# Optimization experiments

Measured on AMD Instinct MI355X. Metric: run time of the kernel, lower is better.

Reference implementation:

```python
import jax, jax.numpy as jnp
import numpy as np

B, N, DEG = 64, 512, 16        # graphs, nodes per graph, avg degree
C, HID = 10, 128               # input feat dim (== num_classes quirk), hidden
E = B * N * DEG                # total edges (fixed; pooling masks edges)


def _gcn(x, W, b, src, dst, emask, n):
    # PyG GCNConv: add self-loops, symmetric norm D^-1/2 (A+I) D^-1/2 (XW) + b
    h = x @ W
    deg = jax.ops.segment_sum(emask, dst, num_segments=n) + 1.0  # +1 self-loop
    dinv = jax.lax.rsqrt(deg)
    norm = dinv[src] * dinv[dst] * emask
    agg = jax.ops.segment_sum(h[src] * norm[:, None], dst, num_segments=n)
    return agg + h * (dinv * dinv)[:, None] + b  # self-loop term + bias


def _sag_pool(x, src, dst, emask, Wp, bp, n_per):
    # SAGPooling: score = tanh(GCN(x)); per-graph top-k (ratio=0.5); x' = x[perm]*score
    n = x.shape[0]
    score = jnp.tanh(_gcn(x, Wp, bp, src, dst, emask, n)[:, 0])
    k = n_per // 2
    vals, idx = jax.lax.top_k(score.reshape(B, n_per), k)  # [B,k]
    perm = (idx + (jnp.arange(B) * n_per)[:, None]).reshape(-1)
    xk = x[perm] * vals.reshape(-1)[:, None]
    # relabel edges; drop edges touching removed nodes via mask (fixed E)
    mapping = jnp.full((n,), -1, jnp.int32).at[perm].set(
        jnp.arange(B * k, dtype=jnp.int32))
    ns, nd = mapping[src], mapping[dst]
    nmask = emask * ((ns >= 0) & (nd >= 0)).astype(emask.dtype)
    return xk, jnp.maximum(ns, 0), jnp.maximum(nd, 0), nmask, k


def _readout(x, k):
    # global max pool || global mean pool (all kept nodes are real, no padding)
    xg = x.reshape(B, k, -1)
    return jnp.concatenate([xg.max(axis=1), xg.mean(axis=1)], axis=1)


def setup_inputs() -> dict:
    key = jax.random.key(0)
    ks = jax.random.split(key, 16)
    x = jax.random.normal(ks[0], (B * N, C), jnp.float32)
    off = jnp.repeat(jnp.arange(B, dtype=jnp.int32) * N, N * DEG)
    src = jax.random.randint(ks[1], (E,), 0, N, jnp.int32) + off
    dst = jax.random.randint(ks[2], (E,), 0, N, jnp.int32) + off
    p = lambda k, s: jax.random.normal(k, s, jnp.float32) * 0.05
    return {
        "x": x, "src": src, "dst": dst,
        "W1": p(ks[3], (C, HID)), "b1": jnp.zeros((HID,), jnp.float32),
        "W2": p(ks[4], (HID, HID)), "b2": jnp.zeros((HID,), jnp.float32),
        "W3": p(ks[5], (HID, HID)), "b3": jnp.zeros((HID,), jnp.float32),
        "Wp": p(ks[6], (HID, 1)), "bp": jnp.zeros((1,), jnp.float32),
        "L1W": p(ks[7], (2 * HID, HID)), "L1b": jnp.zeros((HID,), jnp.float32),
        "L2W": p(ks[8], (HID, HID // 2)), "L2b": jnp.zeros((HID // 2,), jnp.float32),
    }


def reference(x, src, dst, W1, b1, W2, b2, W3, b3, Wp, bp, L1W, L1b, L2W, L2b):
    emask = jnp.ones((E,), jnp.float32)
    h = jax.nn.relu(_gcn(x, W1, b1, src, dst, emask, B * N))
    h, src, dst, emask, k = _sag_pool(h, src, dst, emask, Wp, bp, N)
    x1 = _readout(h, k)
    h = jax.nn.relu(_gcn(h, W2, b2, src, dst, emask, B * k))
    h, src, dst, emask, k = _sag_pool(h, src, dst, emask, Wp, bp, k)
    x2 = _readout(h, k)
    h = jax.nn.relu(_gcn(h, W3, b3, src, dst, emask, B * k))
    h, src, dst, emask, k = _sag_pool(h, src, dst, emask, Wp, bp, k)
    x3 = _readout(h, k)
    z = x1 + x2 + x3
    z = jax.nn.relu(z @ L1W + L1b)
    # dropout inactive in eval mode
    z = jax.nn.relu(z @ L2W + L2b)
    return jax.nn.log_softmax(z, axis=1)
```

## Files before the change

kernel.cpp:

```cpp
#include <hip/hip_runtime.h>
#include <math.h>

#define BGR 64
#define N0 512
#define NDEG 16
#define E_TOT (BGR*N0*NDEG)
#define EPG (N0*NDEG)
#define EIT (EPG/512)
#define HID 128


__global__ __launch_bounds__(512) void k_topo0(
    const int* __restrict__ s0, const int* __restrict__ d0,
    int2* __restrict__ edges, int* __restrict__ cnt, int* __restrict__ rowptr,
    float* __restrict__ dinv, int2* __restrict__ csr, float* __restrict__ z){
  __shared__ int   deg[512];
  __shared__ int   sb[512];
  __shared__ int   cur[512];
  __shared__ float dl[512];
  int g = (blockIdx.x & 7)*8 + (blockIdx.x >> 3);
  int t = threadIdx.x;
  int gbase = g*N0, ebase = g*EPG;
  deg[t] = 0;
  if (t < 256) z[g*256 + t] = 0.f;
  __syncthreads();
  int2 ebuf[EIT];
  #pragma unroll
  for (int it = 0; it < EIT; it++){
    int i = ebase + it*512 + t;
    int2 e = make_int2(s0[i], d0[i]);
    ebuf[it] = e;
    edges[i] = e;
    atomicAdd(&deg[e.y - gbase], 1);
  }
  __syncthreads();
  int vdeg = deg[t];
  sb[t] = vdeg; __syncthreads();
  for (int off = 1; off < 512; off <<= 1){
    int add = (t >= off) ? sb[t-off] : 0;
    __syncthreads(); sb[t] += add; __syncthreads();
  }
  int excl = sb[t] - vdeg;
  rowptr[gbase + t] = ebase + excl;
  cnt[gbase + t] = vdeg;
  cur[t] = excl;
  float dv = rsqrtf((float)vdeg + 1.f);
  dl[t] = dv;
  dinv[gbase + t] = dv;
  __syncthreads();
  #pragma unroll
  for (int it = 0; it < EIT; it++){
    int2 e = ebuf[it];
    int sl = e.x - gbase, dc = e.y - gbase;
    int pos = atomicAdd(&cur[dc], 1);
    csr[ebase + pos] = make_int2(e.x, __float_as_int(dl[sl]*dl[dc]));
  }
}

__global__ __launch_bounds__(512) void k_l1_fused(
    const float* __restrict__ x, const float* __restrict__ W1,
    const int2* __restrict__ csr, const int* __restrict__ rowptr,
    const int* __restrict__ cnt, const float* __restrict__ dinv,
    const float* __restrict__ b1, const float* __restrict__ Wp,
    float4* __restrict__ gout4, float* __restrict__ hp_part){
  extern __shared__ float hl[];
  int b = blockIdx.x;
  int xcd = b & 7, idx = b >> 3;
  int graph = xcd*8 + (idx >> 2);
  int qf = idx & 3;
  int t = threadIdx.x;
  int gbase = graph*N0;
  int fp = t & 31;
  int f = qf*32 + fp;
  float wcol[10];
  #pragma unroll
  for (int k = 0; k < 10; k++) wcol[k] = W1[k*HID + f];
  for (int n = t >> 5; n < N0; n += 16){
    const float* xr = x + (gbase + n)*10;
    float acc = 0.f;
    #pragma unroll
    for (int k = 0; k < 10; k++) acc += xr[k]*wcol[k];
    hl[n*32 + fp] = acc;
  }
  __syncthreads();
  const float4* hl4 = (const float4*)hl;
  int l = t & 7, grp = t >> 3;
  float4 bb = ((const float4*)b1)[qf*8 + l];
  float4 wp = ((const float4*)Wp)[qf*8 + l];
  for (int nl = grp; nl < N0; nl += 64){
    int node = gbase + nl;
    int start = rowptr[node], c = cnt[node];
    float4 acc = make_float4(0.f,0.f,0.f,0.f);
    for (int j = 0; j < c; j++){
      int2 e = csr[start + j];
      float wgt = __int_as_float(e.y);
      float4 hv = hl4[(e.x - gbase)*8 + l];
      acc.x += wgt*hv.x; acc.y += wgt*hv.y; acc.z += wgt*hv.z; acc.w += wgt*hv.w;
    }
    float di = dinv[node], dd = di*di;
    float4 hs = hl4[nl*8 + l];
    float4 v;
    v.x = fmaxf(acc.x + hs.x*dd + bb.x, 0.f);
    v.y = fmaxf(acc.y + hs.y*dd + bb.y, 0.f);
    v.z = fmaxf(acc.z + hs.z*dd + bb.z, 0.f);
    v.w = fmaxf(acc.w + hs.w*dd + bb.w, 0.f);
    gout4[node*32 + qf*8 + l] = v;
    float contrib = v.x*wp.x + v.y*wp.y + v.z*wp.z + v.w*wp.w;
    #pragma unroll
    for (int off = 4; off; off >>= 1) contrib += __shfl_down(contrib, off, 8);
    if (l == 0) hp_part[qf*32768 + node] = contrib;
  }
}

__global__ void k_gemm8(const float* __restrict__ x, const float* __restrict__ W,
                        float* __restrict__ out, int fin, int nper){
  __shared__ float xr[8][HID];
  int b = blockIdx.x;
  int xcd = b & 7, idx = b >> 3, bpg = nper >> 3;
  int graph = xcd*8 + idx / bpg;
  int base = graph*nper + (idx % bpg)*8;
  int f = threadIdx.x;
  #pragma unroll
  for (int nd = 0; nd < 8; nd++) if (f < fin) xr[nd][f] = x[(base+nd)*fin + f];
  __syncthreads();
  float acc[8] = {0,0,0,0,0,0,0,0};
  for (int i = 0; i < fin; i++){
    float wv = W[i*HID + f];
    #pragma unroll
    for (int nd = 0; nd < 8; nd++) acc[nd] += xr[nd][i]*wv;
  }
  #pragma unroll
  for (int nd = 0; nd < 8; nd++) out[(base+nd)*HID + f] = acc[nd];
}

__global__ __launch_bounds__(256) void k_gcn_gather(
    const float4* __restrict__ h4, const int2* __restrict__ csr,
    const int* __restrict__ rowptr, const int* __restrict__ cnt,
    const float* __restrict__ dinv, const float4* __restrict__ bias4,
    const float4* __restrict__ Wp4, float4* __restrict__ out4,
    float* __restrict__ hp, int nper){
  int b = blockIdx.x;
  int xcd = b & 7, idx = b >> 3, bpg = nper >> 3;
  int graph = xcd*8 + idx / bpg;
  int node = graph*nper + (idx % bpg)*8 + (threadIdx.x >> 5);
  int l = threadIdx.x & 31;
  int start = rowptr[node], c = cnt[node];
  float4 acc = make_float4(0.f, 0.f, 0.f, 0.f);
  for (int j = 0; j < c; j++){
    int2 e = csr[start + j];
    float wgt = __int_as_float(e.y);
    float4 hv = h4[e.x*32 + l];
    acc.x += wgt*hv.x; acc.y += wgt*hv.y; acc.z += wgt*hv.z; acc.w += wgt*hv.w;
  }
  float di = dinv[node], dd = di*di;
  float4 hs = h4[node*32 + l];
  float4 bb = bias4[l];
  float4 v;
  v.x = fmaxf(acc.x + hs.x*dd + bb.x, 0.f);
  v.y = fmaxf(acc.y + hs.y*dd + bb.y, 0.f);
  v.z = fmaxf(acc.z + hs.z*dd + bb.z, 0.f);
  v.w = fmaxf(acc.w + hs.w*dd + bb.w, 0.f);
  out4[node*32 + l] = v;
  float4 wp = Wp4[l];
  float contrib = v.x*wp.x + v.y*wp.y + v.z*wp.z + v.w*wp.w;
  #pragma unroll
  for (int off = 16; off; off >>= 1) contrib += __shfl_down(contrib, off, 32);
  if (l == 0) hp[node] = contrib;
}

__global__ __launch_bounds__(512) void k_mega(
    const float4* __restrict__ gout4, const float* __restrict__ hp,
    const float* __restrict__ hp_part, int l1flag,
    int2* __restrict__ csr, int* __restrict__ rowptr, int* __restrict__ cnt,
    float* __restrict__ dinv, const float* __restrict__ bp,
    int2* __restrict__ edges, float4* __restrict__ xpool4,
    float* __restrict__ z, int nper, int lastlev,
    const float* __restrict__ L1W, const float* __restrict__ L1b,
    const float* __restrict__ L2W, const float* __restrict__ L2b,
    float* __restrict__ out){
  __shared__ float sv[512];
  __shared__ int   si[512];
  __shared__ float hpl[512];
  __shared__ int   map[512];
  __shared__ int   sb[512];
  __shared__ int   cur[256];
  __shared__ float dl[256];
  __shared__ float4 pmx[16][32];
  __shared__ float4 psm[16][32];
  __shared__ float zr[256];
  __shared__ float h1[128];
  __shared__ float h2[64];
  __shared__ float red[2];
  int g = (blockIdx.x & 7)*8 + (blockIdx.x >> 3);
  int t = threadIdx.x;
  int k = nper >> 1;
  int gbase = g*nper, ebase = g*EPG, gb2 = g*k;
  bool act = t < nper;
  if (act){
    int node = gbase + t;
    hpl[t] = l1flag ? (hp_part[node] + hp_part[32768 + node] +
                       hp_part[65536 + node] + hp_part[98304 + node])
                    : hp[node];
  }
  __syncthreads();
  float v = 0.f; int idx = t;
  if (act){
    int start = rowptr[gbase + t], c = cnt[gbase + t];
    float a = 0.f;
    for (int j = 0; j < c; j++){
      int2 e = csr[start + j];
      a += __int_as_float(e.y) * hpl[e.x - gbase];
    }
    float di = dinv[gbase + t];
    v = tanhf(a + hpl[t]*di*di + bp[0]);
  }
  for (int kk = 2; kk <= nper; kk <<= 1){
    for (int jj = kk >> 1; jj > 0; jj >>= 1){
      if (jj >= 64){
        if (act){ sv[t] = v; si[t] = idx; }
        __syncthreads();
        if (act){
          int p = t ^ jj;
          float pv = sv[p]; int pi = si[p];
          bool amLower = (t & jj) == 0;
          bool dirDesc = (t & kk) == 0;
          bool betterMine = (v > pv) || (v == pv && idx < pi);
          if ((amLower == dirDesc) != betterMine){ v = pv; idx = pi; }
        }
        __syncthreads();
      } else if (act){
        float pv = __shfl_xor(v, jj);
        int   pi = __shfl_xor(idx, jj);
        bool amLower = (t & jj) == 0;
        bool dirDesc = (t & kk) == 0;
        bool betterMine = (v > pv) || (v == pv && idx < pi);
        if ((amLower == dirDesc) != betterMine){ v = pv; idx = pi; }
      }
    }
  }
  if (act){ sv[t] = v; si[t] = idx; }
  __syncthreads();
  int l = t & 31, j0 = t >> 5;
  float4 mx = make_float4(-INFINITY,-INFINITY,-INFINITY,-INFINITY);
  float4 sm = make_float4(0.f,0.f,0.f,0.f);
  for (int j = j0; j < k; j += 16){
    float val = sv[j]; int row = si[j];
    float4 hv = gout4[(gbase + row)*32 + l];
    float4 o = make_float4(hv.x*val, hv.y*val, hv.z*val, hv.w*val);
    xpool4[(gb2 + j)*32 + l] = o;
    mx.x = fmaxf(mx.x, o.x); mx.y = fmaxf(mx.y, o.y);
    mx.z = fmaxf(mx.z, o.z); mx.w = fmaxf(mx.w, o.w);
    sm.x += o.x; sm.y += o.y; sm.z += o.z; sm.w += o.w;
  }
  pmx[j0][l] = mx; psm[j0][l] = sm;
  __syncthreads();
  if (t < 32){
    float4 M = pmx[0][t], S = psm[0][t];
    #pragma unroll
    for (int q = 1; q < 16; q++){
      float4 m2 = pmx[q][t], s2 = psm[q][t];
      M.x = fmaxf(M.x, m2.x); M.y = fmaxf(M.y, m2.y);
      M.z = fmaxf(M.z, m2.z); M.w = fmaxf(M.w, m2.w);
      S.x += s2.x; S.y += s2.y; S.z += s2.z; S.w += s2.w;
    }
    float ki = 1.f/(float)k;
    float* zp = z + g*256;
    if (!lastlev){
      zp[t*4+0] += M.x; zp[t*4+1] += M.y; zp[t*4+2] += M.z; zp[t*4+3] += M.w;
      zp[128+t*4+0] += S.x*ki; zp[128+t*4+1] += S.y*ki;
      zp[128+t*4+2] += S.z*ki; zp[128+t*4+3] += S.w*ki;
    } else {
      zr[t*4+0] = zp[t*4+0] + M.x; zr[t*4+1] = zp[t*4+1] + M.y;
      zr[t*4+2] = zp[t*4+2] + M.z; zr[t*4+3] = zp[t*4+3] + M.w;
      zr[128+t*4+0] = zp[128+t*4+0] + S.x*ki;
      zr[128+t*4+1] = zp[128+t*4+1] + S.y*ki;
      zr[128+t*4+2] = zp[128+t*4+2] + S.z*ki;
      zr[128+t*4+3] = zp[128+t*4+3] + S.w*ki;
    }
  }
  if (lastlev){
    __syncthreads();
    if (t < 128){
      float a = L1b[t];
      for (int i = 0; i < 256; i++) a += zr[i]*L1W[i*128 + t];
      h1[t] = fmaxf(a, 0.f);
    }
    __syncthreads();
    if (t < 64){
      float a = L2b[t];
      for (int i = 0; i < 128; i++) a += h1[i]*L2W[i*64 + t];
      h2[t] = fmaxf(a, 0.f);
    }
    __syncthreads();
    if (t == 0){
      float mxv = -INFINITY;
      for (int i = 0; i < 64; i++) mxv = fmaxf(mxv, h2[i]);
      float s = 0.f;
      for (int i = 0; i < 64; i++) s += expf(h2[i] - mxv);
      red[0] = mxv; red[1] = logf(s);
    }
    __syncthreads();
    if (t < 64) out[g*64 + t] = h2[t] - red[0] - red[1];
    return;
  }
  if (act) map[t] = -1;
  if (t < k) sb[t] = 0;
  __syncthreads();
  if (t < k) map[si[t]] = t;
  __syncthreads();
  int2 ebuf[EIT];
  #pragma unroll
  for (int it = 0; it < EIT; it++){
    int i = ebase + it*512 + t;
    int2 e = edges[i];
    int2 ne = make_int2(-1, 0);
    if (e.x >= 0){
      int ns = map[e.x - gbase], nd = map[e.y - gbase];
      if (ns >= 0 && nd >= 0){
        ne = make_int2(gb2 + ns, gb2 + nd);
        atomicAdd(&sb[nd], 1);
      }
    }
    ebuf[it] = ne;
    edges[i] = ne;
  }
  __syncthreads();
  int vdeg = (t < k) ? sb[t] : 0;
  for (int off = 1; off < k; off <<= 1){
    int add = (t >= off && t < k) ? sb[t-off] : 0;
    __syncthreads();
    if (t < k) sb[t] += add;
    __syncthreads();
  }
  if (t < k){
    int excl = sb[t] - vdeg;
    rowptr[gb2 + t] = ebase + excl;
    cnt[gb2 + t] = vdeg;
    cur[t] = excl;
    float dv = rsqrtf((float)vdeg + 1.f);
    dl[t] = dv;
    dinv[gb2 + t] = dv;
  }
  __syncthreads();
  #pragma unroll
  for (int it = 0; it < EIT; it++){
    int2 e = ebuf[it];
    if (e.x >= 0){
      int sl = e.x - gb2, dc = e.y - gb2;
      int pos = atomicAdd(&cur[dc], 1);
      csr[ebase + pos] = make_int2(e.x, __float_as_int(dl[sl]*dl[dc]));
    }
  }
}

extern "C" void kernel_launch(void* const* d_in, const int* in_sizes, int n_in,
                              void* d_out, int out_size, void* d_ws, size_t ws_size,
                              hipStream_t stream){
  (void)in_sizes; (void)n_in; (void)out_size; (void)ws_size;
  const float* x0  = (const float*)d_in[0];
  const int*   s0  = (const int*)  d_in[1];
  const int*   d0  = (const int*)  d_in[2];
  const float* W1  = (const float*)d_in[3];  const float* b1 = (const float*)d_in[4];
  const float* W2  = (const float*)d_in[5];  const float* b2 = (const float*)d_in[6];
  const float* W3  = (const float*)d_in[7];  const float* b3 = (const float*)d_in[8];
  const float* Wp  = (const float*)d_in[9];  const float* bp = (const float*)d_in[10];
  const float* L1W = (const float*)d_in[11]; const float* L1b = (const float*)d_in[12];
  const float* L2W = (const float*)d_in[13]; const float* L2b = (const float*)d_in[14];
  float* out = (float*)d_out;

  float* w = (float*)d_ws;
  float* h     = w; w += 32768*HID;
  float* gout  = w; w += 32768*HID;
  float* xpA   = h    + 16384*HID;
  float* xpB   = gout + 16384*HID;
  float* xpC   = xpA;
  float* dinvv = w; w += 32768;
  float* hp    = w; w += 32768;
  float* hppt  = w; w += 4*32768;
  float* z     = w; w += BGR*256;
  int* cnt     = (int*)w; w += 32768;
  int* rowptr  = (int*)w; w += 32768;
  int2* edges  = (int2*)w; w += E_TOT*2;
  int2* csr    = (int2*)w; w += E_TOT*2;

  k_topo0<<<BGR, 512, 0, stream>>>(s0, d0, edges, cnt, rowptr, dinvv, csr, z);

  k_l1_fused<<<256, 512, 65536, stream>>>(x0, W1, csr, rowptr, cnt, dinvv,
                                          b1, Wp, (float4*)gout, hppt);
  k_mega<<<BGR, 512, 0, stream>>>((const float4*)gout, hp, hppt, 1, csr, rowptr,
                                  cnt, dinvv, bp, edges, (float4*)xpA, z, 512, 0,
                                  L1W, L1b, L2W, L2b, out);
  k_gemm8<<<16384/8, HID, 0, stream>>>(xpA, W2, h, HID, 256);
  k_gcn_gather<<<16384/8, 256, 0, stream>>>((const float4*)h, csr, rowptr, cnt, dinvv,
                                            (const float4*)b2, (const float4*)Wp,
                                            (float4*)gout, hp, 256);
  k_mega<<<BGR, 512, 0, stream>>>((const float4*)gout, hp, hppt, 0, csr, rowptr,
                                  cnt, dinvv, bp, edges, (float4*)xpB, z, 256, 0,
                                  L1W, L1b, L2W, L2b, out);
  k_gemm8<<<8192/8, HID, 0, stream>>>(xpB, W3, h, HID, 128);
  k_gcn_gather<<<8192/8, 256, 0, stream>>>((const float4*)h, csr, rowptr, cnt, dinvv,
                                           (const float4*)b3, (const float4*)Wp,
                                           (float4*)gout, hp, 128);
  k_mega<<<BGR, 512, 0, stream>>>((const float4*)gout, hp, hppt, 0, csr, rowptr,
                                  cnt, dinvv, bp, edges, (float4*)xpC, z, 128, 1,
                                  L1W, L1b, L2W, L2b, out);
}
```

Baseline: 254.5 us.

## Fuse layer-2/3 GEMM and GCN gather into per-graph-quarter kernel with LDS-resident features

Replaces the separate k_gemm8 and k_gcn_gather launches for layers 2 and 3 with one k_lx_fused kernel. Each block handles one graph and one quarter of the feature columns, keeps the W slice and the transformed node features in shared memory, and does the neighbour gather from LDS instead of global memory. The pooling-score dot product is written as four partial sums that k_mega adds, matching layer 1. Pooled features are no longer stored at the last level. This removes kernel launches and a global round trip of the hidden features, at the cost of only 256 blocks and redundant reads of x across the four column-quarter blocks.

```diff
diff --git a/kernel.cpp b/kernel.cpp
--- a/kernel.cpp
+++ b/kernel.cpp
@@ -3,10 +3,9 @@
 
 #define BGR 64
 #define N0 512
-#define NDEG 16
-#define E_TOT (BGR*N0*NDEG)
-#define EPG (N0*NDEG)
-#define EIT (EPG/512)
+#define E_TOT (BGR*N0*16)
+#define EPG 8192
+#define EIT 16
 #define HID 128
 
 
@@ -112,65 +111,67 @@
   }
 }
 
-__global__ void k_gemm8(const float* __restrict__ x, const float* __restrict__ W,
-                        float* __restrict__ out, int fin, int nper){
-  __shared__ float xr[8][HID];
+__global__ __launch_bounds__(512) void k_lx_fused(
+    const float* __restrict__ x, const float* __restrict__ W,
+    const int2* __restrict__ csr, const int* __restrict__ rowptr,
+    const int* __restrict__ cnt, const float* __restrict__ dinv,
+    const float* __restrict__ bia, const float* __restrict__ Wp,
+    float4* __restrict__ gout4, float* __restrict__ hp_part, int nper){
+  extern __shared__ float smem[];
+  float* wl = smem;
+  float* hl = smem + 4096;
   int b = blockIdx.x;
-  int xcd = b & 7, idx = b >> 3, bpg = nper >> 3;
-  int graph = xcd*8 + idx / bpg;
-  int base = graph*nper + (idx % bpg)*8;
-  int f = threadIdx.x;
-  #pragma unroll
-  for (int nd = 0; nd < 8; nd++) if (f < fin) xr[nd][f] = x[(base+nd)*fin + f];
-  __syncthreads();
-  float acc[8] = {0,0,0,0,0,0,0,0};
-  for (int i = 0; i < fin; i++){
-    float wv = W[i*HID + f];
+  int xcd = b & 7, idx = b >> 3;
+  int graph = xcd*8 + (idx >> 2);
+  int qf = idx & 3;
+  int t = threadIdx.x;
+  int gbase = graph*nper;
+  int fp = t & 31, f = qf*32 + fp;
+  for (int kk = t >> 5; kk < 128; kk += 16) wl[kk*32 + fp] = W[kk*HID + f];
+  __syncthreads();
+  for (int n = t >> 5; n < nper; n += 16){
+    const float4* xr = (const float4*)(x + (gbase + n)*HID);
+    float acc = 0.f;
+    #pragma unroll 8
+    for (int kk = 0; kk < 32; kk++){
+      float4 xv = xr[kk];
+      acc += xv.x*wl[(kk*4+0)*32 + fp] + xv.y*wl[(kk*4+1)*32 + fp]
+           + xv.z*wl[(kk*4+2)*32 + fp] + xv.w*wl[(kk*4+3)*32 + fp];
+    }
+    hl[n*32 + fp] = acc;
+  }
+  __syncthreads();
+  const float4* hl4 = (const float4*)hl;
+  int l = t & 7, grp = t >> 3;
+  float4 bb = ((const float4*)bia)[qf*8 + l];
+  float4 wp = ((const float4*)Wp)[qf*8 + l];
+  for (int nl = grp; nl < nper; nl += 64){
+    int node = gbase + nl;
+    int start = rowptr[node], c = cnt[node];
+    float4 acc = make_float4(0.f,0.f,0.f,0.f);
+    for (int j = 0; j < c; j++){
+      int2 e = csr[start + j];
+      float wgt = __int_as_float(e.y);
+      float4 hv = hl4[(e.x - gbase)*8 + l];
+      acc.x += wgt*hv.x; acc.y += wgt*hv.y; acc.z += wgt*hv.z; acc.w += wgt*hv.w;
+    }
+    float di = dinv[node], dd = di*di;
+    float4 hs = hl4[nl*8 + l];
+    float4 v;
+    v.x = fmaxf(acc.x + hs.x*dd + bb.x, 0.f);
+    v.y = fmaxf(acc.y + hs.y*dd + bb.y, 0.f);
+    v.z = fmaxf(acc.z + hs.z*dd + bb.z, 0.f);
+    v.w = fmaxf(acc.w + hs.w*dd + bb.w, 0.f);
+    gout4[node*32 + qf*8 + l] = v;
+    float contrib = v.x*wp.x + v.y*wp.y + v.z*wp.z + v.w*wp.w;
     #pragma unroll
-    for (int nd = 0; nd < 8; nd++) acc[nd] += xr[nd][i]*wv;
-  }
-  #pragma unroll
-  for (int nd = 0; nd < 8; nd++) out[(base+nd)*HID + f] = acc[nd];
+    for (int off = 4; off; off >>= 1) contrib += __shfl_down(contrib, off, 8);
+    if (l == 0) hp_part[qf*32768 + node] = contrib;
+  }
 }
 
-__global__ __launch_bounds__(256) void k_gcn_gather(
-    const float4* __restrict__ h4, const int2* __restrict__ csr,
-    const int* __restrict__ rowptr, const int* __restrict__ cnt,
-    const float* __restrict__ dinv, const float4* __restrict__ bias4,
-    const float4* __restrict__ Wp4, float4* __restrict__ out4,
-    float* __restrict__ hp, int nper){
-  int b = blockIdx.x;
-  int xcd = b & 7, idx = b >> 3, bpg = nper >> 3;
-  int graph = xcd*8 + idx / bpg;
-  int node = graph*nper + (idx % bpg)*8 + (threadIdx.x >> 5);
-  int l = threadIdx.x & 31;
-  int start = rowptr[node], c = cnt[node];
-  float4 acc = make_float4(0.f, 0.f, 0.f, 0.f);
-  for (int j = 0; j < c; j++){
-    int2 e = csr[start + j];
-    float wgt = __int_as_float(e.y);
-    float4 hv = h4[e.x*32 + l];
-    acc.x += wgt*hv.x; acc.y += wgt*hv.y; acc.z += wgt*hv.z; acc.w += wgt*hv.w;
-  }
-  float di = dinv[node], dd = di*di;
-  float4 hs = h4[node*32 + l];
-  float4 bb = bias4[l];
-  float4 v;
-  v.x = fmaxf(acc.x + hs.x*dd + bb.x, 0.f);
-  v.y = fmaxf(acc.y + hs.y*dd + bb.y, 0.f);
-  v.z = fmaxf(acc.z + hs.z*dd + bb.z, 0.f);
-  v.w = fmaxf(acc.w + hs.w*dd + bb.w, 0.f);
-  out4[node*32 + l] = v;
-  float4 wp = Wp4[l];
-  float contrib = v.x*wp.x + v.y*wp.y + v.z*wp.z + v.w*wp.w;
-  #pragma unroll
-  for (int off = 16; off; off >>= 1) contrib += __shfl_down(contrib, off, 32);
-  if (l == 0) hp[node] = contrib;
-}
-
 __global__ __launch_bounds__(512) void k_mega(
-    const float4* __restrict__ gout4, const float* __restrict__ hp,
-    const float* __restrict__ hp_part, int l1flag,
+    const float4* __restrict__ gout4, const float* __restrict__ hp_part,
     int2* __restrict__ csr, int* __restrict__ rowptr, int* __restrict__ cnt,
     float* __restrict__ dinv, const float* __restrict__ bp,
     int2* __restrict__ edges, float4* __restrict__ xpool4,
@@ -198,9 +199,8 @@
   bool act = t < nper;
   if (act){
     int node = gbase + t;
-    hpl[t] = l1flag ? (hp_part[node] + hp_part[32768 + node] +
-                       hp_part[65536 + node] + hp_part[98304 + node])
-                    : hp[node];
+    hpl[t] = hp_part[node] + hp_part[32768 + node]
+           + hp_part[65536 + node] + hp_part[98304 + node];
   }
   __syncthreads();
   float v = 0.f; int idx = t;
@@ -247,7 +247,7 @@
     float val = sv[j]; int row = si[j];
     float4 hv = gout4[(gbase + row)*32 + l];
     float4 o = make_float4(hv.x*val, hv.y*val, hv.z*val, hv.w*val);
-    xpool4[(gb2 + j)*32 + l] = o;
+    if (!lastlev) xpool4[(gb2 + j)*32 + l] = o;
     mx.x = fmaxf(mx.x, o.x); mx.y = fmaxf(mx.y, o.y);
     mx.z = fmaxf(mx.z, o.z); mx.w = fmaxf(mx.w, o.w);
     sm.x += o.x; sm.y += o.y; sm.z += o.z; sm.w += o.w;
@@ -369,39 +369,34 @@
   float* out = (float*)d_out;
 
   float* w = (float*)d_ws;
-  float* h     = w; w += 32768*HID;
   float* gout  = w; w += 32768*HID;
-  float* xpA   = h    + 16384*HID;
-  float* xpB   = gout + 16384*HID;
-  float* xpC   = xpA;
+  float* xpA   = w; w += 16384*HID;
+  float* xpB   = w; w += 8192*HID;
   float* dinvv = w; w += 32768;
-  float* hp    = w; w += 32768;
   float* hppt  = w; w += 4*32768;
   float* z     = w; w += BGR*256;
   int* cnt     = (int*)w; w += 32768;
   int* rowptr  = (int*)w; w += 32768;
-  int2* edges  = (int2*)w; w += E_TOT*2;
-  int2* csr    = (int2*)w; w += E_TOT*2;
+  int2* edges  = (int2*)w; w += 2*E_TOT;
+  int2* csr    = (int2*)w; w += 2*E_TOT;
 
   k_topo0<<<BGR, 512, 0, stream>>>(s0, d0, edges, cnt, rowptr, dinvv, csr, z);
 
   k_l1_fused<<<256, 512, 65536, stream>>>(x0, W1, csr, rowptr, cnt, dinvv,
                                           b1, Wp, (float4*)gout, hppt);
-  k_mega<<<BGR, 512, 0, stream>>>((const float4*)gout, hp, hppt, 1, csr, rowptr,
-                                  cnt, dinvv, bp, edges, (float4*)xpA, z, 512, 0,
+  k_mega<<<BGR, 512, 0, stream>>>((const float4*)gout, hppt, csr, rowptr, cnt,
+                                  dinvv, bp, edges, (float4*)xpA, z, 512, 0,
                                   L1W, L1b, L2W, L2b, out);
-  k_gemm8<<<16384/8, HID, 0, stream>>>(xpA, W2, h, HID, 256);
-  k_gcn_gather<<<16384/8, 256, 0, stream>>>((const float4*)h, csr, rowptr, cnt, dinvv,
-                                            (const float4*)b2, (const float4*)Wp,
-                                            (float4*)gout, hp, 256);
-  k_mega<<<BGR, 512, 0, stream>>>((const float4*)gout, hp, hppt, 0, csr, rowptr,
-                                  cnt, dinvv, bp, edges, (float4*)xpB, z, 256, 0,
+  k_lx_fused<<<256, 512, (4096 + 256*32)*4, stream>>>(xpA, W2, csr, rowptr, cnt,
+                                                      dinvv, b2, Wp, (float4*)gout,
+                                                      hppt, 256);
+  k_mega<<<BGR, 512, 0, stream>>>((const float4*)gout, hppt, csr, rowptr, cnt,
+                                  dinvv, bp, edges, (float4*)xpB, z, 256, 0,
                                   L1W, L1b, L2W, L2b, out);
-  k_gemm8<<<8192/8, HID, 0, stream>>>(xpB, W3, h, HID, 128);
-  k_gcn_gather<<<8192/8, 256, 0, stream>>>((const float4*)h, csr, rowptr, cnt, dinvv,
-                                           (const float4*)b3, (const float4*)Wp,
-                                           (float4*)gout, hp, 128);
-  k_mega<<<BGR, 512, 0, stream>>>((const float4*)gout, hp, hppt, 0, csr, rowptr,
-                                  cnt, dinvv, bp, edges, (float4*)xpC, z, 128, 1,
+  k_lx_fused<<<256, 512, (4096 + 128*32)*4, stream>>>(xpB, W3, csr, rowptr, cnt,
+                                                      dinvv, b3, Wp, (float4*)gout,
+                                                      hppt, 128);
+  k_mega<<<BGR, 512, 0, stream>>>((const float4*)gout, hppt, csr, rowptr, cnt,
+                                  dinvv, bp, edges, (float4*)xpA, z, 128, 1,
                                   L1W, L1b, L2W, L2b, out);
 }
```

After: 301.5 us. +18.5%, slower.
